# Optimization experiments

Measured on AMD Instinct MI355X. Metric: run time of the kernel, lower is better.

Reference implementation:

```python
import jax, jax.numpy as jnp
import numpy as np

B, N = 2, 256
NODE_DIM, EDGE_DIM, HID, H = 128, 256, 256, 8
D = HID // H
LN_EPS = 1e-5


def _layernorm(x, g, b):
    m = jnp.mean(x, axis=-1, keepdims=True)
    v = jnp.mean((x - m) ** 2, axis=-1, keepdims=True)
    return (x - m) * jax.lax.rsqrt(v + LN_EPS) * g + b


def setup_inputs() -> dict:
    key = jax.random.key(0)
    ks = iter(jax.random.split(key, 32))

    def w(i, o):
        return jax.random.normal(next(ks), (i, o), jnp.float32) * 0.02

    inp = {
        "node_features": jax.random.normal(next(ks), (B, N, NODE_DIM), jnp.float32),
        "edge_features": jax.random.normal(next(ks), (B, N, N, EDGE_DIM), jnp.float32),
        "adj_mask": jax.random.randint(next(ks), (B, N, N), 0, 2, jnp.int32),
        "Wn": w(NODE_DIM, HID), "bn": jnp.zeros((HID,), jnp.float32),
        "Wq": w(HID, HID), "bq": jnp.zeros((HID,), jnp.float32),
        "Wk": w(HID, HID), "bk": jnp.zeros((HID,), jnp.float32),
        "Wv": w(HID, HID), "bv": jnp.zeros((HID,), jnp.float32),
        "Wep": w(EDGE_DIM, HID), "bep": jnp.zeros((HID,), jnp.float32),
        "Weg": w(EDGE_DIM, HID), "beg": jnp.zeros((HID,), jnp.float32),
        "Wo": w(HID, HID), "bo": jnp.zeros((HID,), jnp.float32),
        "Weo": w(HID, EDGE_DIM), "beo": jnp.zeros((EDGE_DIM,), jnp.float32),
        "g1": jnp.ones((HID,), jnp.float32), "b1": jnp.zeros((HID,), jnp.float32),
        "g2": jnp.ones((EDGE_DIM,), jnp.float32), "b2": jnp.zeros((EDGE_DIM,), jnp.float32),
    }
    return inp


def reference(node_features, edge_features, adj_mask,
              Wn, bn, Wq, bq, Wk, bk, Wv, bv,
              Wep, bep, Weg, beg, Wo, bo, Weo, beo,
              g1, b1, g2, b2):
    # node projection -> residual
    h = node_features @ Wn + bn                      # [B,N,HID]
    residual = h

    # multi-head Q/K/V: [B,H,N,D]
    def heads(x):
        return x.reshape(B, N, H, D).transpose(0, 2, 1, 3)

    Q, K, V = heads(h @ Wq + bq), heads(h @ Wk + bk), heads(h @ Wv + bv)

    scores = jnp.einsum('bhnd,bhmd->bhnm', Q, K) / np.sqrt(D).astype(np.float32)

    # edge bias: gated sum over head_dim -> [B,H,N,N]
    edge_h = (edge_features @ Wep + bep).reshape(B, N, N, H, D)
    edge_gate = jax.nn.sigmoid(edge_features @ Weg + beg).reshape(B, N, N, H, D)
    edge_attn = jnp.einsum('bnmhd,bnmhd->bhnm', edge_h, edge_gate)

    scores = scores + edge_attn
    mask = (adj_mask == 0)[:, None, :, :]            # [B,1,N,N]
    scores = jnp.where(mask, jnp.float32(-1e9), scores)
    attn = jax.nn.softmax(scores, axis=-1)           # [B,H,N,N]

    attn_out = jnp.einsum('bhnm,bhmd->bhnd', attn, V)
    attn_out = attn_out.transpose(0, 2, 1, 3).reshape(B, N, HID)

    h_out = _layernorm(residual + (attn_out @ Wo + bo), g1, b1)

    # edge update: mean attention over heads * pairwise node-feature mean
    attn_mean = jnp.mean(attn, axis=1)               # [B,N,N]
    pair = 0.5 * (h_out[:, :, None, :] + h_out[:, None, :, :])  # [B,N,N,HID]
    edge_update = attn_mean[..., None] * pair
    edge_out = _layernorm(edge_features + (edge_update @ Weo + beo), g2, b2)

    return (h_out, edge_out)
```

## Files before the change

### kernel.cpp

```cpp
#include <hip/hip_runtime.h>
#include <hip/hip_bf16.h>

#define BB 2
#define NN 256
#define HID 256
#define NH 8
#define HD 32
#define NPAIR (BB*NN*NN)

typedef __attribute__((ext_vector_type(8))) short bf16x8;
typedef __attribute__((ext_vector_type(4))) float f32x4;

__device__ __forceinline__ unsigned short f2bf(float f){
  union{float f; unsigned int i;} v; v.f=f;
  unsigned int r = v.i + 0x7fffu + ((v.i>>16)&1u);
  return (unsigned short)(r>>16);
}

__device__ __forceinline__ float block_reduce_sum(float v, float* red){
  int t = threadIdx.x;
  red[t]=v; __syncthreads();
  for(int off=128; off>0; off>>=1){ if(t<off) red[t]+=red[t+off]; __syncthreads(); }
  float r = red[0]; __syncthreads();
  return r;
}

__global__ void k_build_w(const float* __restrict__ Wep,
                          const float* __restrict__ bep,
                          const float* __restrict__ Weg,
                          const float* __restrict__ beg,
                          unsigned short* __restrict__ WcatT,
                          float* __restrict__ bcat){
  int vcol = blockIdx.x, k = threadIdx.x;
  int hv = vcol >> 6, wi = vcol & 63;
  int col = hv*32 + (wi & 31);
  const float* W = (wi < 32) ? Wep : Weg;
  WcatT[(size_t)vcol*256 + k] = f2bf(W[(size_t)k*256 + col]);
  if (k==0){
    const float* bb = (wi<32) ? bep : beg;
    bcat[vcol] = bb[col];
  }
}

__global__ __launch_bounds__(256) void k_nodeqkv(
    const float* __restrict__ node, const float* __restrict__ Wn,
    const float* __restrict__ bn,
    const float* __restrict__ Wq, const float* __restrict__ bq,
    const float* __restrict__ Wk, const float* __restrict__ bk,
    const float* __restrict__ Wv, const float* __restrict__ bv,
    float* __restrict__ h,
    float* __restrict__ Q, float* __restrict__ K, float* __restrict__ V){
  __shared__ float xs[128];
  __shared__ float hs[256];
  int row = blockIdx.x, c = threadIdx.x;
  if (c < 128) xs[c] = node[(size_t)row*128 + c];
  __syncthreads();
  float acc = bn[c];
#pragma unroll 16
  for (int k=0;k<128;k++) acc += xs[k]*Wn[(size_t)k*256+c];
  h[(size_t)row*256+c] = acc;
  hs[c] = acc;
  __syncthreads();
  float aq = bq[c], ak = bk[c], av = bv[c];
#pragma unroll 16
  for (int k=0;k<256;k++){
    float x = hs[k];
    aq += x*Wq[(size_t)k*256+c];
    ak += x*Wk[(size_t)k*256+c];
    av += x*Wv[(size_t)k*256+c];
  }
  Q[(size_t)row*256+c]=aq; K[(size_t)row*256+c]=ak; V[(size_t)row*256+c]=av;
}

__global__ __launch_bounds__(256) void k_edge_gemm(
    const float* __restrict__ edge,
    const unsigned short* __restrict__ WcatT,
    const float* __restrict__ bcat,
    float* __restrict__ edge_attn)
{
  __shared__ __align__(16) short As[128][72];
  __shared__ __align__(16) short Bs[128][72];
  int id = blockIdx.x;
  int bm = ((id>>5)<<3) | (id&7);
  int bv = (id>>3)&3;
  int tid = threadIdx.x;
  int w = tid>>6, lane = tid&63;
  int wr = w>>1, wc = w&1;
  int q = lane>>4, cl = lane&15;

  f32x4 acc[4][4];
#pragma unroll
  for(int i=0;i<4;i++)
#pragma unroll
    for(int j=0;j<4;j++) acc[i][j] = (f32x4){0.f,0.f,0.f,0.f};

  int r0 = tid>>4, c4 = tid&15;
  for(int kc=0;kc<4;kc++){
    int k0 = kc*64;
#pragma unroll
    for(int i=0;i<8;i++){
      int r = r0 + i*16;
      float4 f = *(const float4*)(edge + (size_t)(bm*128+r)*256 + k0 + c4*4);
      __hip_bfloat162 lo = __float22bfloat162_rn(make_float2(f.x,f.y));
      __hip_bfloat162 hi = __float22bfloat162_rn(make_float2(f.z,f.w));
      uint2 u; u.x = *(unsigned int*)&lo; u.y = *(unsigned int*)&hi;
      *(uint2*)(&As[r][c4*4]) = u;
    }
#pragma unroll
    for(int i=0;i<4;i++){
      int g = tid + i*256; int r = g>>3, s8 = g&7;
      *(uint4*)(&Bs[r][s8*8]) = *(const uint4*)(WcatT + (size_t)(bv*128+r)*256 + k0 + s8*8);
    }
    __syncthreads();
#pragma unroll
    for(int ks=0;ks<2;ks++){
      int kb = ks*32 + q*8;
      bf16x8 a[4], bfr[4];
#pragma unroll
      for(int tm=0;tm<4;tm++) a[tm]  = *(const bf16x8*)(&As[wr*64+tm*16+cl][kb]);
#pragma unroll
      for(int tn=0;tn<4;tn++) bfr[tn]= *(const bf16x8*)(&Bs[wc*64+tn*16+cl][kb]);
#pragma unroll
      for(int tm=0;tm<4;tm++)
#pragma unroll
        for(int tn=0;tn<4;tn++)
          acc[tm][tn] = __builtin_amdgcn_mfma_f32_16x16x32_bf16(a[tm], bfr[tn], acc[tm][tn], 0, 0, 0);
    }
    __syncthreads();
  }

  int head = bv*2 + wc;
  float bias[4];
#pragma unroll
  for(int tn=0;tn<4;tn++) bias[tn] = bcat[bv*128 + wc*64 + tn*16 + cl];

#pragma unroll
  for(int tm=0;tm<4;tm++){
    float s[4] = {0.f,0.f,0.f,0.f};
#pragma unroll
    for(int tn=0;tn<2;tn++){
#pragma unroll
      for(int r=0;r<4;r++){
        float eh = acc[tm][tn][r]   + bias[tn];
        float gg = acc[tm][tn+2][r] + bias[tn+2];
        s[r] += eh * (1.f/(1.f + __expf(-gg)));
      }
    }
#pragma unroll
    for(int off=1;off<16;off<<=1){
#pragma unroll
      for(int r=0;r<4;r++) s[r] += __shfl_xor(s[r], off);
    }
    if (cl==0){
      int R = bm*128 + wr*64 + tm*16 + q*4;
      int b = R>>16, rem = R&65535;
#pragma unroll
      for(int r=0;r<4;r++)
        edge_attn[(size_t)(b*NH+head)*65536 + rem + r] = s[r];
    }
  }
}

__global__ __launch_bounds__(256) void k_attn(
    const float* __restrict__ Q, const float* __restrict__ Km,
    const float* __restrict__ V, const int* __restrict__ adj,
    float* __restrict__ attn, float* __restrict__ attn_out){
  __shared__ float Ks[256][33];
  __shared__ float Vs[256][33];
  __shared__ float arow[4][264];
  int b = blockIdx.z, hh = blockIdx.y;
  int t = threadIdx.x;
  int mrow = t>>3, dg = (t&7)*4;
#pragma unroll
  for(int it=0; it<8; it++){
    int m = mrow + it*32;
    size_t base = ((size_t)(b*NN+m))*HID + hh*HD + dg;
    *(float4*)&Ks[m][dg] = *(const float4*)(Km + base);
    *(float4*)&Vs[m][dg] = *(const float4*)(V + base);
  }
  __syncthreads();

  int w = t>>6, lane = t&63;
  int n = blockIdx.x*4 + w;
  const float* qp = Q + ((size_t)(b*NN+n))*HID + hh*HD;
  float4 q[8];
#pragma unroll
  for(int i=0;i<8;i++) q[i] = *(const float4*)(qp + i*4);

  size_t eoff = ((size_t)((b*NH+hh)*NN + n))*NN;
  const int* abase = adj + ((size_t)(b*NN+n))*NN;
  float sc[4];
#pragma unroll
  for(int j=0;j<4;j++){
    int m = lane + j*64;
    float d = 0.f;
#pragma unroll
    for(int i=0;i<8;i++){
      float4 kk = *(float4*)&Ks[m][i*4];
      d += q[i].x*kk.x + q[i].y*kk.y + q[i].z*kk.z + q[i].w*kk.w;
    }
    float s = d*0.17677669529663687f + attn[eoff + m];
    if (abase[m]==0) s = -1e9f;
    sc[j] = s;
  }
  float mx = fmaxf(fmaxf(sc[0],sc[1]),fmaxf(sc[2],sc[3]));
#pragma unroll
  for(int off=1;off<64;off<<=1) mx = fmaxf(mx, __shfl_xor(mx, off));
  float e[4], sum = 0.f;
#pragma unroll
  for(int j=0;j<4;j++){ e[j] = __expf(sc[j]-mx); sum += e[j]; }
#pragma unroll
  for(int off=1;off<64;off<<=1) sum += __shfl_xor(sum, off);
  float inv = 1.f/sum;
#pragma unroll
  for(int j=0;j<4;j++){
    int m = lane + j*64;
    float a = e[j]*inv;
    attn[eoff + m] = a;
    arow[w][m + (m>>5)] = a;
  }
  int mc = lane>>3, dg4 = (lane&7)*4;
  float4 o = {0.f,0.f,0.f,0.f};
#pragma unroll
  for(int j=0;j<32;j++){
    int m = mc*32 + j;
    float a = arow[w][m + (m>>5)];
    float4 v = *(float4*)&Vs[m][dg4];
    o.x += a*v.x; o.y += a*v.y; o.z += a*v.z; o.w += a*v.w;
  }
#pragma unroll
  for(int off=8; off<64; off<<=1){
    o.x += __shfl_xor(o.x, off); o.y += __shfl_xor(o.y, off);
    o.z += __shfl_xor(o.z, off); o.w += __shfl_xor(o.w, off);
  }
  if (mc==0)
    *(float4*)(attn_out + ((size_t)(b*NN+n))*HID + hh*HD + dg4) = o;
}

__global__ void k_attn_mean(const float* __restrict__ attn, float* __restrict__ am){
  int p = blockIdx.x*256 + threadIdx.x;
  int b = p>>16, rem = p&65535;
  float s = 0.f;
#pragma unroll
  for(int hh=0; hh<NH; hh++) s += attn[(size_t)(b*NH+hh)*65536 + rem];
  am[p] = s*0.125f;
}

__global__ __launch_bounds__(256) void k_hout(
    const float* __restrict__ attn_out, const float* __restrict__ hres,
    const float* __restrict__ Wo, const float* __restrict__ bo,
    const float* __restrict__ g1, const float* __restrict__ b1,
    const float* __restrict__ Weo,
    float* __restrict__ P, float* __restrict__ out){
  __shared__ float xs[256]; __shared__ float red[256]; __shared__ float hs[256];
  int row = blockIdx.x, c = threadIdx.x;
  xs[c] = attn_out[(size_t)row*256 + c];
  __syncthreads();
  float acc = bo[c];
#pragma unroll 16
  for(int k=0;k<256;k++) acc += xs[k]*Wo[(size_t)k*256+c];
  float val = hres[(size_t)row*256+c] + acc;
  float mean = block_reduce_sum(val, red) * (1.f/256.f);
  float ctr = val - mean;
  float var = block_reduce_sum(ctr*ctr, red) * (1.f/256.f);
  float o = ctr * rsqrtf(var + 1e-5f) * g1[c] + b1[c];
  out[(size_t)row*256+c] = o;
  hs[c] = o;
  __syncthreads();
  float accP = 0.f;
#pragma unroll 16
  for(int k=0;k<256;k++) accP += hs[k]*Weo[(size_t)k*256+c];
  P[(size_t)row*256+c] = accP;
}

__global__ __launch_bounds__(256) void k_edge_out(
    const float* __restrict__ ef, const float* __restrict__ am,
    const float* __restrict__ P, const float* __restrict__ beo,
    const float* __restrict__ g2, const float* __restrict__ b2,
    float* __restrict__ out){
  int w = threadIdx.x>>6, lane = threadIdx.x&63;
  size_t pair = (size_t)blockIdx.x*4 + w;
  int b = (int)(pair>>16); int rem = (int)(pair&65535);
  int n = rem>>8, m = rem&255;
  float a = am[pair]*0.5f;
  const float* Pn = P + (size_t)(b*NN+n)*HID;
  const float* Pm = P + (size_t)(b*NN+m)*HID;
  int c0 = lane*4;
  float4 ev = *(const float4*)(ef + pair*256 + c0);
  float4 pn = *(const float4*)(Pn + c0);
  float4 pm = *(const float4*)(Pm + c0);
  float4 bo4 = *(const float4*)(beo + c0);
  float v0 = ev.x + a*(pn.x+pm.x) + bo4.x;
  float v1 = ev.y + a*(pn.y+pm.y) + bo4.y;
  float v2 = ev.z + a*(pn.z+pm.z) + bo4.z;
  float v3 = ev.w + a*(pn.w+pm.w) + bo4.w;
  float s = v0+v1+v2+v3;
#pragma unroll
  for(int off=1;off<64;off<<=1) s += __shfl_xor(s, off);
  float mean = s*(1.f/256.f);
  float c0f=v0-mean, c1f=v1-mean, c2f=v2-mean, c3f=v3-mean;
  float sq = c0f*c0f+c1f*c1f+c2f*c2f+c3f*c3f;
#pragma unroll
  for(int off=1;off<64;off<<=1) sq += __shfl_xor(sq, off);
  float rs = rsqrtf(sq*(1.f/256.f) + 1e-5f);
  float4 g = *(const float4*)(g2 + c0);
  float4 bb = *(const float4*)(b2 + c0);
  float4 o;
  o.x = c0f*rs*g.x+bb.x;
  o.y = c1f*rs*g.y+bb.y;
  o.z = c2f*rs*g.z+bb.z;
  o.w = c3f*rs*g.w+bb.w;
  *(float4*)(out + pair*256 + c0) = o;
}

extern "C" void kernel_launch(void* const* d_in, const int* in_sizes, int n_in,
                              void* d_out, int out_size, void* d_ws, size_t ws_size,
                              hipStream_t stream){
  (void)in_sizes; (void)n_in; (void)out_size; (void)ws_size;
  const float* node = (const float*)d_in[0];
  const float* edge = (const float*)d_in[1];
  const int*   adj  = (const int*)d_in[2];
  const float* Wn  = (const float*)d_in[3];
  const float* bn  = (const float*)d_in[4];
  const float* Wq  = (const float*)d_in[5];
  const float* bq  = (const float*)d_in[6];
  const float* Wk  = (const float*)d_in[7];
  const float* bk  = (const float*)d_in[8];
  const float* Wv  = (const float*)d_in[9];
  const float* bv  = (const float*)d_in[10];
  const float* Wep = (const float*)d_in[11];
  const float* bep = (const float*)d_in[12];
  const float* Weg = (const float*)d_in[13];
  const float* beg = (const float*)d_in[14];
  const float* Wo  = (const float*)d_in[15];
  const float* bo  = (const float*)d_in[16];
  const float* Weo = (const float*)d_in[17];
  const float* beo = (const float*)d_in[18];
  const float* g1  = (const float*)d_in[19];
  const float* b1  = (const float*)d_in[20];
  const float* g2  = (const float*)d_in[21];
  const float* b2  = (const float*)d_in[22];

  unsigned short* WcatT = (unsigned short*)d_ws;
  float* fws  = (float*)((char*)d_ws + (size_t)512*256*2);
  float* bcat = fws;
  float* h    = bcat + 512;
  float* Q    = h    + 131072;
  float* K    = Q    + 131072;
  float* V    = K    + 131072;
  float* attn = V    + 131072;
  float* am   = attn + 1048576;
  float* P    = am   + 131072;
  float* aout = P    + 131072;

  float* out = (float*)d_out;

  k_build_w  <<<512, 256, 0, stream>>>(Wep, bep, Weg, beg, WcatT, bcat);
  k_nodeqkv  <<<512, 256, 0, stream>>>(node, Wn, bn, Wq, bq, Wk, bk, Wv, bv, h, Q, K, V);
  k_edge_gemm<<<4096, 256, 0, stream>>>(edge, WcatT, bcat, attn);
  k_attn     <<<dim3(64,8,2), 256, 0, stream>>>(Q, K, V, adj, attn, aout);
  k_attn_mean<<<512, 256, 0, stream>>>(attn, am);
  k_hout     <<<512, 256, 0, stream>>>(aout, h, Wo, bo, g1, b1, Weo, P, out);
  k_edge_out <<<32768, 256, 0, stream>>>(edge, am, P, beo, g2, b2, out + (size_t)BB*NN*HID);
}
```

Before: 391.6 us.

## Register-prefetch next K-chunk in edge GEMM and fuse head-mean into edge_out

The edge GEMM kernel now loads the next 64-wide K chunk of the edge features and the weights into registers while MFMAs run on the current shared-memory tile. This overlaps global latency with compute at the cost of more registers. Separately, the attn_mean kernel is removed and k_edge_out sums the 8 head attention values per pair itself. That drops one launch and an intermediate buffer but makes each wave issue 8 scalar broadcast loads.

```diff
diff --git a/kernel.cpp b/kernel.cpp
--- a/kernel.cpp
+++ b/kernel.cpp
@@ -95,23 +95,35 @@
     for(int j=0;j<4;j++) acc[i][j] = (f32x4){0.f,0.f,0.f,0.f};
 
   int r0 = tid>>4, c4 = tid&15;
+  const float* aRow = edge + (size_t)(bm*128 + r0)*256 + c4*4;
+  const unsigned short* bRow = WcatT + (size_t)(bv*128 + (tid>>3))*256 + (tid&7)*8;
+
+  float4 fA[8]; uint4 uB[4];
+#pragma unroll
+  for(int i=0;i<8;i++) fA[i] = *(const float4*)(aRow + (size_t)i*16*256);
+#pragma unroll
+  for(int i=0;i<4;i++) uB[i] = *(const uint4*)(bRow + (size_t)i*32*256);
+
   for(int kc=0;kc<4;kc++){
-    int k0 = kc*64;
 #pragma unroll
     for(int i=0;i<8;i++){
-      int r = r0 + i*16;
-      float4 f = *(const float4*)(edge + (size_t)(bm*128+r)*256 + k0 + c4*4);
+      float4 f = fA[i];
       __hip_bfloat162 lo = __float22bfloat162_rn(make_float2(f.x,f.y));
       __hip_bfloat162 hi = __float22bfloat162_rn(make_float2(f.z,f.w));
       uint2 u; u.x = *(unsigned int*)&lo; u.y = *(unsigned int*)&hi;
-      *(uint2*)(&As[r][c4*4]) = u;
-    }
-#pragma unroll
-    for(int i=0;i<4;i++){
-      int g = tid + i*256; int r = g>>3, s8 = g&7;
-      *(uint4*)(&Bs[r][s8*8]) = *(const uint4*)(WcatT + (size_t)(bv*128+r)*256 + k0 + s8*8);
-    }
+      *(uint2*)(&As[r0 + i*16][c4*4]) = u;
+    }
+#pragma unroll
+    for(int i=0;i<4;i++)
+      *(uint4*)(&Bs[(tid>>3) + i*32][(tid&7)*8]) = uB[i];
     __syncthreads();
+    if (kc<3){
+      int k1 = (kc+1)*64;
+#pragma unroll
+      for(int i=0;i<8;i++) fA[i] = *(const float4*)(aRow + (size_t)i*16*256 + k1);
+#pragma unroll
+      for(int i=0;i<4;i++) uB[i] = *(const uint4*)(bRow + (size_t)i*32*256 + k1);
+    }
 #pragma unroll
     for(int ks=0;ks<2;ks++){
       int kb = ks*32 + q*8;
@@ -237,15 +249,6 @@
     *(float4*)(attn_out + ((size_t)(b*NN+n))*HID + hh*HD + dg4) = o;
 }
 
-__global__ void k_attn_mean(const float* __restrict__ attn, float* __restrict__ am){
-  int p = blockIdx.x*256 + threadIdx.x;
-  int b = p>>16, rem = p&65535;
-  float s = 0.f;
-#pragma unroll
-  for(int hh=0; hh<NH; hh++) s += attn[(size_t)(b*NH+hh)*65536 + rem];
-  am[p] = s*0.125f;
-}
-
 __global__ __launch_bounds__(256) void k_hout(
     const float* __restrict__ attn_out, const float* __restrict__ hres,
     const float* __restrict__ Wo, const float* __restrict__ bo,
@@ -274,7 +277,7 @@
 }
 
 __global__ __launch_bounds__(256) void k_edge_out(
-    const float* __restrict__ ef, const float* __restrict__ am,
+    const float* __restrict__ ef, const float* __restrict__ attn,
     const float* __restrict__ P, const float* __restrict__ beo,
     const float* __restrict__ g2, const float* __restrict__ b2,
     float* __restrict__ out){
@@ -282,7 +285,11 @@
   size_t pair = (size_t)blockIdx.x*4 + w;
   int b = (int)(pair>>16); int rem = (int)(pair&65535);
   int n = rem>>8, m = rem&255;
-  float a = am[pair]*0.5f;
+  const float* ap = attn + (size_t)b*NH*65536 + rem;
+  float ssum = 0.f;
+#pragma unroll
+  for(int hh=0; hh<NH; hh++) ssum += ap[(size_t)hh*65536];
+  float a = ssum * 0.0625f;
   const float* Pn = P + (size_t)(b*NN+n)*HID;
   const float* Pm = P + (size_t)(b*NN+m)*HID;
   int c0 = lane*4;
@@ -359,7 +366,6 @@
   k_nodeqkv  <<<512, 256, 0, stream>>>(node, Wn, bn, Wq, bq, Wk, bk, Wv, bv, h, Q, K, V);
   k_edge_gemm<<<4096, 256, 0, stream>>>(edge, WcatT, bcat, attn);
   k_attn     <<<dim3(64,8,2), 256, 0, stream>>>(Q, K, V, adj, attn, aout);
-  k_attn_mean<<<512, 256, 0, stream>>>(attn, am);
   k_hout     <<<512, 256, 0, stream>>>(aout, h, Wo, bo, g1, b1, Weo, P, out);
-  k_edge_out <<<32768, 256, 0, stream>>>(edge, am, P, beo, g2, b2, out + (size_t)BB*NN*HID);
-}
+  k_edge_out <<<32768, 256, 0, stream>>>(edge, attn, P, beo, g2, b2, out + (size_t)BB*NN*HID);
+}
```

After: 469.6 us. 1.2x slower.

## Double-buffer edge tile in LDS and read weights directly from global

Applied to the files above, without the earlier changes.

Restructures the edge GEMM main loop to use a double-buffered A tile of 32-wide K steps, prefetching the next fp32 edge chunk into registers while the MFMAs run on the current buffer. The B (weight) fragments are loaded straight from global memory instead of being staged through shared memory. Launch bounds now request 4 blocks per SM. Together these are meant to hide global load latency and cut LDS use and barriers per K step. The cost is more barriers overall (8 K steps instead of 4) and uncoalesced per-lane global weight loads that rely on cache hits.

```diff
diff --git a/kernel.cpp b/kernel.cpp
--- a/kernel.cpp
+++ b/kernel.cpp
@@ -72,14 +72,13 @@
   Q[(size_t)row*256+c]=aq; K[(size_t)row*256+c]=ak; V[(size_t)row*256+c]=av;
 }
 
-__global__ __launch_bounds__(256) void k_edge_gemm(
+__global__ __launch_bounds__(256, 4) void k_edge_gemm(
     const float* __restrict__ edge,
     const unsigned short* __restrict__ WcatT,
     const float* __restrict__ bcat,
     float* __restrict__ edge_attn)
 {
-  __shared__ __align__(16) short As[128][72];
-  __shared__ __align__(16) short Bs[128][72];
+  __shared__ __align__(16) short As[2][128][40];
   int id = blockIdx.x;
   int bm = ((id>>5)<<3) | (id&7);
   int bv = (id>>3)&3;
@@ -94,40 +93,61 @@
 #pragma unroll
     for(int j=0;j<4;j++) acc[i][j] = (f32x4){0.f,0.f,0.f,0.f};
 
-  int r0 = tid>>4, c4 = tid&15;
-  for(int kc=0;kc<4;kc++){
-    int k0 = kc*64;
-#pragma unroll
-    for(int i=0;i<8;i++){
-      int r = r0 + i*16;
-      float4 f = *(const float4*)(edge + (size_t)(bm*128+r)*256 + k0 + c4*4);
-      __hip_bfloat162 lo = __float22bfloat162_rn(make_float2(f.x,f.y));
-      __hip_bfloat162 hi = __float22bfloat162_rn(make_float2(f.z,f.w));
-      uint2 u; u.x = *(unsigned int*)&lo; u.y = *(unsigned int*)&hi;
-      *(uint2*)(&As[r][c4*4]) = u;
-    }
-#pragma unroll
-    for(int i=0;i<4;i++){
-      int g = tid + i*256; int r = g>>3, s8 = g&7;
-      *(uint4*)(&Bs[r][s8*8]) = *(const uint4*)(WcatT + (size_t)(bv*128+r)*256 + k0 + s8*8);
+  int r0 = tid>>3, grp4 = (tid&7)*4;
+  const float* aP = edge + (size_t)(bm*128 + r0)*256 + grp4;
+
+  {
+    float4 f0 = *(const float4*)(aP);
+    float4 f1 = *(const float4*)(aP + 32*256);
+    float4 f2 = *(const float4*)(aP + 64*256);
+    float4 f3 = *(const float4*)(aP + 96*256);
+#define CVT_WR(BUF,ROW,F) { \
+    __hip_bfloat162 lo_ = __float22bfloat162_rn(make_float2((F).x,(F).y)); \
+    __hip_bfloat162 hi_ = __float22bfloat162_rn(make_float2((F).z,(F).w)); \
+    uint2 u_; u_.x = *(unsigned int*)&lo_; u_.y = *(unsigned int*)&hi_; \
+    *(uint2*)(&As[BUF][ROW][grp4]) = u_; }
+    CVT_WR(0, r0,      f0);
+    CVT_WR(0, r0+32,   f1);
+    CVT_WR(0, r0+64,   f2);
+    CVT_WR(0, r0+96,   f3);
+  }
+  __syncthreads();
+
+  const unsigned short* bP = WcatT + (size_t)(bv*128 + wc*64 + cl)*256 + q*8;
+
+  for (int kt=0; kt<8; ++kt){
+    int cur = kt&1;
+    bool pf = (kt < 7);
+    float4 f0,f1,f2,f3;
+    if (pf){
+      int k1 = (kt+1)*32;
+      f0 = *(const float4*)(aP + k1);
+      f1 = *(const float4*)(aP + 32*256 + k1);
+      f2 = *(const float4*)(aP + 64*256 + k1);
+      f3 = *(const float4*)(aP + 96*256 + k1);
+    }
+    bf16x8 bfr[4], a[4];
+#pragma unroll
+    for(int tn=0;tn<4;tn++)
+      bfr[tn] = *(const bf16x8*)(bP + (size_t)tn*4096 + kt*32);
+#pragma unroll
+    for(int tm=0;tm<4;tm++)
+      a[tm] = *(const bf16x8*)(&As[cur][wr*64 + tm*16 + cl][q*8]);
+#pragma unroll
+    for(int tm=0;tm<4;tm++)
+#pragma unroll
+      for(int tn=0;tn<4;tn++)
+        acc[tm][tn] = __builtin_amdgcn_mfma_f32_16x16x32_bf16(a[tm], bfr[tn], acc[tm][tn], 0, 0, 0);
+    if (pf){
+      int nb = cur^1;
+      CVT_WR(nb, r0,      f0);
+      CVT_WR(nb, r0+32,   f1);
+      CVT_WR(nb, r0+64,   f2);
+      CVT_WR(nb, r0+96,   f3);
     }
     __syncthreads();
-#pragma unroll
-    for(int ks=0;ks<2;ks++){
-      int kb = ks*32 + q*8;
-      bf16x8 a[4], bfr[4];
-#pragma unroll
-      for(int tm=0;tm<4;tm++) a[tm]  = *(const bf16x8*)(&As[wr*64+tm*16+cl][kb]);
-#pragma unroll
-      for(int tn=0;tn<4;tn++) bfr[tn]= *(const bf16x8*)(&Bs[wc*64+tn*16+cl][kb]);
-#pragma unroll
-      for(int tm=0;tm<4;tm++)
-#pragma unroll
-        for(int tn=0;tn<4;tn++)
-          acc[tm][tn] = __builtin_amdgcn_mfma_f32_16x16x32_bf16(a[tm], bfr[tn], acc[tm][tn], 0, 0, 0);
-    }
-    __syncthreads();
-  }
+  }
+#undef CVT_WR
 
   int head = bv*2 + wc;
   float bias[4];
```

Result: slower. 455.4 us (+16.3%).
